# Kernel tuning notes

Hardware: AMD Instinct MI355X
Metric: run time of the kernel (lower is better)

The kernel has to match this reference:

```python
import jax, jax.numpy as jnp
import numpy as np

H = 128          # hidden_dim
L = 4            # num_layers
NUM_RBF = 16
CUTOFF = 10.0
TIME_DIM = 64
B, N = 4, 512


def _lin_init(key, din, dout):
    return jax.random.normal(key, (din, dout), dtype=jnp.float32) * 0.02


def setup_inputs() -> dict:
    key = jax.random.key(0)
    ks = jax.random.split(key, 16)
    x = jax.random.normal(ks[0], (B, N, 3), dtype=jnp.float32) * 3.0  # spread distances over RBF range
    t = jax.random.uniform(ks[1], (B,), dtype=jnp.float32) * 1000.0
    din_msg = 2 * H + NUM_RBF  # 272
    inp = {
        "x": x,
        "t": t,
        "time_w1": _lin_init(ks[2], TIME_DIM, H),
        "time_b1": jnp.zeros((H,), jnp.float32),
        "time_w2": _lin_init(ks[3], H, H),
        "time_b2": jnp.zeros((H,), jnp.float32),
        # stacked per-layer params, leading axis = layer
        "msg_w1": jax.random.normal(ks[4], (L, din_msg, H), jnp.float32) * 0.02,
        "msg_b1": jnp.zeros((L, H), jnp.float32),
        "msg_w2": jax.random.normal(ks[5], (L, H, H), jnp.float32) * 0.02,
        "msg_b2": jnp.zeros((L, H), jnp.float32),
        "cw1": jax.random.normal(ks[6], (L, H, H), jnp.float32) * 0.02,
        "cb1": jnp.zeros((L, H), jnp.float32),
        "cw2": jax.random.normal(ks[7], (L, H, 1), jnp.float32) * 0.02,
        "cb2": jnp.zeros((L, 1), jnp.float32),
    }
    return inp


def _time_embed(t):
    half = TIME_DIM // 2
    freqs = jnp.exp(jnp.arange(half, dtype=jnp.float32) * (-np.log(10000.0) / (half - 1)))
    ang = t[:, None] * freqs[None, :]                    # (B, half)
    return jnp.concatenate([jnp.sin(ang), jnp.cos(ang)], axis=-1)  # (B, TIME_DIM)


def reference(x, t, time_w1, time_b1, time_w2, time_b2,
              msg_w1, msg_b1, msg_w2, msg_b2, cw1, cb1, cw2, cb2):
    silu = jax.nn.silu
    b, n = x.shape[0], x.shape[1]

    te = _time_embed(t)
    t_emb = silu(te @ time_w1 + time_b1) @ time_w2 + time_b2      # (B, H)
    h = jnp.broadcast_to(t_emb[:, None, :], (b, n, H))            # (B, N, H)

    centers = jnp.linspace(0.0, CUTOFF, NUM_RBF)
    width = CUTOFF / NUM_RBF
    coord_updates = jnp.zeros_like(x)

    for l in range(L):
        diff = x[:, None, :, :] - x[:, :, None, :]                # (B,N,N,3), x_j - x_i
        dist = jnp.linalg.norm(diff, axis=-1)                     # (B,N,N)
        edge_mask = (dist < CUTOFF) & (dist > 0)
        rbf = jnp.exp(-((dist[..., None] - centers) ** 2) / (2.0 * width ** 2))  # (B,N,N,R)

        h_i = jnp.broadcast_to(h[:, :, None, :], (b, n, n, H))
        h_j = jnp.broadcast_to(h[:, None, :, :], (b, n, n, H))
        msg_in = jnp.concatenate([h_i, h_j, rbf], axis=-1)        # (B,N,N,2H+R)

        messages = silu(msg_in @ msg_w1[l] + msg_b1[l]) @ msg_w2[l] + msg_b2[l]
        messages = messages * edge_mask[..., None]
        h = h + messages.sum(axis=2)                              # reduce over j

        weights = silu(messages @ cw1[l] + cb1[l]) @ cw2[l] + cb2[l]  # (B,N,N,1)
        weights = weights * edge_mask[..., None]
        directions = diff / (dist[..., None] + 1e-8)
        coord_updates = coord_updates + (weights * directions).sum(axis=2)

    return coord_updates
```

## Files before the change

### kernel.cpp

```cpp
#include <hip/hip_runtime.h>
#include <hip/hip_bf16.h>
#include <math.h>

#define HD 128
#define NN 512
#define BBATCH 4
#define JT 32

typedef __attribute__((ext_vector_type(8))) short bf16x8;
typedef __attribute__((ext_vector_type(4))) float f32x4;
typedef unsigned int uint;
typedef unsigned short ushort;

#define MFMA16 __builtin_amdgcn_mfma_f32_16x16x32_bf16

__device__ __forceinline__ float silu_f(float v) { return v / (1.f + __expf(-v)); }

__device__ __forceinline__ short f2bf(float v) {
    union { __hip_bfloat16 h; short s; } u;
    u.h = __float2bfloat16(v);
    return u.s;
}

__global__ void k_time(const float* __restrict__ t,
                       const float* __restrict__ w1, const float* __restrict__ b1,
                       const float* __restrict__ w2, const float* __restrict__ b2,
                       float* __restrict__ t_emb) {
    int b = blockIdx.x;
    int h = threadIdx.x;
    __shared__ float te[64];
    __shared__ float hid[128];
    float tv = t[b];
    if (h < 32) {
        const float cst = (float)(-2.302585092994046 * 4.0 / 31.0);
        float freq = __expf((float)h * cst);
        float ang = tv * freq;
        te[h]      = sinf(ang);
        te[h + 32] = cosf(ang);
    }
    __syncthreads();
    float acc = b1[h];
    #pragma unroll 8
    for (int k = 0; k < 64; ++k) acc += te[k] * w1[k * HD + h];
    hid[h] = silu_f(acc);
    __syncthreads();
    float acc2 = b2[h];
    #pragma unroll 8
    for (int k = 0; k < HD; ++k) acc2 += hid[k] * w2[k * HD + h];
    t_emb[b * HD + h] = acc2;
}

__global__ void k_bcast(const float* __restrict__ t_emb, float* __restrict__ h,
                        ushort* __restrict__ hb) {
    int idx = blockIdx.x * 256 + threadIdx.x;
    int hch = idx & 127;
    int b = idx >> 16;
    float v = t_emb[b * HD + hch];
    h[idx] = v;
    hb[idx] = (ushort)f2bf(v);
}

__global__ void k_proj(const float* __restrict__ h,
                       const float* __restrict__ w1,
                       const float* __restrict__ b1,
                       float* __restrict__ A) {
    int node = blockIdx.x;
    int hc = threadIdx.x;
    __shared__ float hrow[HD];
    hrow[hc] = h[node * HD + hc];
    __syncthreads();
    float a = b1[hc];
    #pragma unroll 8
    for (int k = 0; k < HD; ++k) a += hrow[k] * w1[k * HD + hc];
    A[node * HD + hc] = a;
}

__global__ __launch_bounds__(256, 2)
void k_edge(const float* __restrict__ x,
            const float* __restrict__ h_in, const ushort* __restrict__ hb_in,
            float* __restrict__ h_out, ushort* __restrict__ hb_out,
            const float* __restrict__ A,
            const float* __restrict__ w1,
            const float* __restrict__ w2,
            const float* __restrict__ b2,
            const float* __restrict__ cw1,
            const float* __restrict__ cb1,
            const float* __restrict__ cw2,
            const float* __restrict__ cb2,
            float* __restrict__ out) {
    __shared__ uint4 sAq[2][JT * 32];
    __shared__ uint4 sMAq[JT * 16];
    __shared__ uint4 sMMq[JT * 16];
    __shared__ __align__(16) float sPart[JT * 68];
    __shared__ float sDir[2][JT][3];
    __shared__ float sMask[2][JT];
    __shared__ float sHS[HD];
    __shared__ float sCA[JT][3];

    const int tid = threadIdx.x;
    const int l  = tid & 63;
    const int w  = tid >> 6;
    const int lg = l >> 4;
    const int ln = l & 15;
    const int nb = w * 32;
    const int n0 = nb + ln;
    const int n1 = n0 + 16;
    const int node = blockIdx.x;
    const int b = node >> 9;
    const float* __restrict__ xb = x + (size_t)b * NN * 3;
    const ushort* __restrict__ hbN = hb_in + (size_t)b * NN * HD;

    const float* w1m = w1 + 128 * HD;
    const float* w1r = w1 + 256 * HD;

    const float bb20 = b2[n0], bb21 = b2[n1];
    const float cb10 = cb1[n0], cb11 = cb1[n1];
    const float cwv0 = cw2[n0], cwv1 = cw2[n1];
    const float cb2v = cb2[0];
    const float xi0 = x[node * 3 + 0], xi1 = x[node * 3 + 1], xi2 = x[node * 3 + 2];
    const float cstep = 10.f / 15.f;
    const float rbfk = 1.28f;

    bf16x8 wM[2][4], w2f[2][4], c1f[2][4], wR[2];
    #pragma unroll
    for (int nt = 0; nt < 2; ++nt) {
        int n = nb + nt * 16 + ln;
        #pragma unroll
        for (int ks = 0; ks < 4; ++ks) {
            #pragma unroll
            for (int i = 0; i < 8; ++i) {
                int k = ks * 32 + lg * 8 + i;
                wM[nt][ks][i]  = f2bf(w1m[k * HD + n]);
                w2f[nt][ks][i] = f2bf(w2[k * HD + n]);
                c1f[nt][ks][i] = f2bf(cw1[k * HD + n]);
            }
        }
        #pragma unroll
        for (int i = 0; i < 8; ++i) {
            int kr = lg * 8 + i;
            float v = (kr < 16) ? w1r[kr * HD + n]
                    : (kr == 16 ? A[node * HD + n] : 0.f);
            wR[nt][i] = f2bf(v);
        }
    }

    if (tid < 64) {
        char* base = (char*)sAq[tid >> 5] + (tid & 31) * 512;
        int sw = ((tid & 7) << 4);
        *(uint*)(base + (288 ^ sw) + 0)  = 0x00003F80u;
        *(uint*)(base + (288 ^ sw) + 4)  = 0u;
        *(uint*)(base + (288 ^ sw) + 8)  = 0u;
        *(uint*)(base + (288 ^ sw) + 12) = 0u;
        uint4 z4 = {0u, 0u, 0u, 0u};
        *(uint4*)(base + (304 ^ sw)) = z4;
    }

    const int hr = tid >> 4, hseg = tid & 15;
    const int jj = tid >> 3, rp = tid & 7;

    {
        char* bufc = (char*)sAq[0];
        const ushort* src = hbN + (size_t)hr * HD + hseg * 8;
        uint4 hv0 = *(const uint4*)src;
        uint4 hv1 = *(const uint4*)(src + 16 * HD);
        const float* xj = xb + jj * 3;
        float d0 = xj[0] - xi0, d1 = xj[1] - xi1, d2 = xj[2] - xi2;
        float d = sqrtf(d0 * d0 + d1 * d1 + d2 * d2);
        float c0 = (float)(rp * 2) * cstep;
        float e0 = __expf(-(d - c0) * (d - c0) * rbfk);
        float e1 = __expf(-(d - c0 - cstep) * (d - c0 - cstep) * rbfk);
        uint pk = (uint)(ushort)f2bf(e0) | ((uint)(ushort)f2bf(e1) << 16);
        *(uint*)(bufc + jj * 512 + ((256 + (rp & 4) * 4) ^ ((jj & 7) << 4)) + (rp & 3) * 4) = pk;
        if (rp == 0) {
            float inv = 1.f / (d + 1e-8f);
            sDir[0][jj][0] = d0 * inv; sDir[0][jj][1] = d1 * inv; sDir[0][jj][2] = d2 * inv;
            sMask[0][jj] = (d < 10.f && d > 0.f) ? 1.f : 0.f;
        }
        int off = (hseg * 16) ^ ((hr & 7) << 4);
        *(uint4*)(bufc + hr * 512 + off) = hv0;
        *(uint4*)(bufc + (hr + 16) * 512 + off) = hv1;
    }
    float hreg0 = 0.f, hreg1 = 0.f;
    float ca0 = 0.f, ca1 = 0.f, ca2 = 0.f;
    __syncthreads();

    const int swA = (ln & 7) << 4;
    const int colb0 = nb * 2 + (ln & 8) * 2 + (ln & 7) * 2;
    const int colb1 = (nb + 16) * 2 + (ln & 8) * 2 + (ln & 7) * 2;

    for (int it = 0; it <= 16; ++it) {
        if (it > 0) {
            const int pm = (it - 1) & 1;
            const char* pp = (const char*)sPart + jj * 272;
            f32x4 pa = *(const f32x4*)(pp + ((jj & 7) << 4 ^ (rp * 32)));
            f32x4 pb = *(const f32x4*)(pp + ((jj & 7) << 4 ^ (rp * 32 + 16)));
            float s = pa[0] + pa[1] + pa[2] + pa[3] + pb[0] + pb[1] + pb[2] + pb[3];
            s += __shfl_xor(s, 1); s += __shfl_xor(s, 2); s += __shfl_xor(s, 4);
            if (rp == 0) {
                float wv = (s + cb2v) * sMask[pm][jj];
                ca0 += wv * sDir[pm][jj][0];
                ca1 += wv * sDir[pm][jj][1];
                ca2 += wv * sDir[pm][jj][2];
            }
        }
        if (it == 16) break;
        const int p = it & 1;

        uint4 hv0, hv1;
        if (it < 15) {
            const ushort* src = hbN + (size_t)((it + 1) * JT + hr) * HD + hseg * 8;
            hv0 = *(const uint4*)src;
            hv1 = *(const uint4*)(src + 16 * HD);
            char* bufn = (char*)sAq[p ^ 1];
            int j = (it + 1) * JT + jj;
            const float* xj = xb + j * 3;
            float d0 = xj[0] - xi0, d1 = xj[1] - xi1, d2 = xj[2] - xi2;
            float d = sqrtf(d0 * d0 + d1 * d1 + d2 * d2);
            float c0 = (float)(rp * 2) * cstep;
            float e0 = __expf(-(d - c0) * (d - c0) * rbfk);
            float e1 = __expf(-(d - c0 - cstep) * (d - c0 - cstep) * rbfk);
            uint pk = (uint)(ushort)f2bf(e0) | ((uint)(ushort)f2bf(e1) << 16);
            *(uint*)(bufn + jj * 512 + ((256 + (rp & 4) * 4) ^ ((jj & 7) << 4)) + (rp & 3) * 4) = pk;
            if (rp == 0) {
                float inv = 1.f / (d + 1e-8f);
                sDir[p ^ 1][jj][0] = d0 * inv; sDir[p ^ 1][jj][1] = d1 * inv; sDir[p ^ 1][jj][2] = d2 * inv;
                sMask[p ^ 1][jj] = (d < 10.f && d > 0.f) ? 1.f : 0.f;
            }
        }

        {
            const char* bufc = (const char*)sAq[p];
            f32x4 zz = {0.f, 0.f, 0.f, 0.f};
            f32x4 pacc[2][2];
            #pragma unroll
            for (int mt = 0; mt < 2; ++mt) {
                pacc[mt][0] = zz; pacc[mt][1] = zz;
                const char* rowp = bufc + (ln + mt * 16) * 512;
                bf16x8 af[5];
                #pragma unroll
                for (int ks = 0; ks < 5; ++ks)
                    af[ks] = *(const bf16x8*)(rowp + ((ks * 64 + lg * 16) ^ swA));
                #pragma unroll
                for (int ks = 0; ks < 4; ++ks) {
                    pacc[mt][0] = MFMA16(af[ks], wM[0][ks], pacc[mt][0], 0, 0, 0);
                    pacc[mt][1] = MFMA16(af[ks], wM[1][ks], pacc[mt][1], 0, 0, 0);
                }
                pacc[mt][0] = MFMA16(af[4], wR[0], pacc[mt][0], 0, 0, 0);
                pacc[mt][1] = MFMA16(af[4], wR[1], pacc[mt][1], 0, 0, 0);
            }
            #pragma unroll
            for (int mt = 0; mt < 2; ++mt)
                #pragma unroll
                for (int reg = 0; reg < 4; ++reg) {
                    int j = mt * 16 + lg * 4 + reg;
                    int sw = (j & 7) << 4;
                    *(short*)((char*)sMAq + j * 256 + (colb0 ^ sw)) = f2bf(silu_f(pacc[mt][0][reg]));
                    *(short*)((char*)sMAq + j * 256 + (colb1 ^ sw)) = f2bf(silu_f(pacc[mt][1][reg]));
                }
        }
        if (it < 15) {
            char* bufn = (char*)sAq[p ^ 1];
            int off = (hseg * 16) ^ ((hr & 7) << 4);
            *(uint4*)(bufn + hr * 512 + off) = hv0;
            *(uint4*)(bufn + (hr + 16) * 512 + off) = hv1;
        }
        __syncthreads();

        {
            f32x4 macc[2][2];
            f32x4 i0 = {bb20, bb20, bb20, bb20};
            f32x4 i1 = {bb21, bb21, bb21, bb21};
            #pragma unroll
            for (int mt = 0; mt < 2; ++mt) {
                macc[mt][0] = i0; macc[mt][1] = i1;
                const char* rowp = (const char*)sMAq + (ln + mt * 16) * 256;
                bf16x8 am[4];
                #pragma unroll
                for (int ks = 0; ks < 4; ++ks)
                    am[ks] = *(const bf16x8*)(rowp + ((ks * 64 + lg * 16) ^ swA));
                #pragma unroll
                for (int ks = 0; ks < 4; ++ks) {
                    macc[mt][0] = MFMA16(am[ks], w2f[0][ks], macc[mt][0], 0, 0, 0);
                    macc[mt][1] = MFMA16(am[ks], w2f[1][ks], macc[mt][1], 0, 0, 0);
                }
            }
            #pragma unroll
            for (int mt = 0; mt < 2; ++mt)
                #pragma unroll
                for (int reg = 0; reg < 4; ++reg) {
                    int j = mt * 16 + lg * 4 + reg;
                    float msk = sMask[p][j];
                    float g0 = macc[mt][0][reg] * msk;
                    float g1 = macc[mt][1][reg] * msk;
                    hreg0 += g0; hreg1 += g1;
                    int sw = (j & 7) << 4;
                    *(short*)((char*)sMMq + j * 256 + (colb0 ^ sw)) = f2bf(g0);
                    *(short*)((char*)sMMq + j * 256 + (colb1 ^ sw)) = f2bf(g1);
                }
        }
        __syncthreads();

        {
            f32x4 cacc[2][2];
            f32x4 i0 = {cb10, cb10, cb10, cb10};
            f32x4 i1 = {cb11, cb11, cb11, cb11};
            #pragma unroll
            for (int mt = 0; mt < 2; ++mt) {
                cacc[mt][0] = i0; cacc[mt][1] = i1;
                const char* rowp = (const char*)sMMq + (ln + mt * 16) * 256;
                bf16x8 am[4];
                #pragma unroll
                for (int ks = 0; ks < 4; ++ks)
                    am[ks] = *(const bf16x8*)(rowp + ((ks * 64 + lg * 16) ^ swA));
                #pragma unroll
                for (int ks = 0; ks < 4; ++ks) {
                    cacc[mt][0] = MFMA16(am[ks], c1f[0][ks], cacc[mt][0], 0, 0, 0);
                    cacc[mt][1] = MFMA16(am[ks], c1f[1][ks], cacc[mt][1], 0, 0, 0);
                }
            }
            #pragma unroll
            for (int mt = 0; mt < 2; ++mt)
                #pragma unroll
                for (int reg = 0; reg < 4; ++reg) {
                    int j = mt * 16 + lg * 4 + reg;
                    float v = silu_f(cacc[mt][0][reg]) * cwv0 + silu_f(cacc[mt][1][reg]) * cwv1;
                    *(float*)((char*)sPart + j * 272 + (((w * 16 + ln) * 4) ^ ((j & 7) << 4))) = v;
                }
        }
        __syncthreads();
    }

    float t0 = hreg0 + __shfl_xor(hreg0, 16); t0 += __shfl_xor(t0, 32);
    float t1 = hreg1 + __shfl_xor(hreg1, 16); t1 += __shfl_xor(t1, 32);
    if (lg == 0) { sHS[n0] = t0; sHS[n1] = t1; }
    if (rp == 0) { sCA[jj][0] = ca0; sCA[jj][1] = ca1; sCA[jj][2] = ca2; }
    __syncthreads();
    if (tid < HD) {
        float hv = h_in[node * HD + tid] + sHS[tid];
        h_out[node * HD + tid] = hv;
        hb_out[node * HD + tid] = (ushort)f2bf(hv);
    }
    if (tid < 3) {
        float s = 0.f;
        #pragma unroll
        for (int q = 0; q < JT; ++q) s += sCA[q][tid];
        out[node * 3 + tid] += s;
    }
}

extern "C" void kernel_launch(void* const* d_in, const int* in_sizes, int n_in,
                              void* d_out, int out_size, void* d_ws, size_t ws_size,
                              hipStream_t stream) {
    const float* x   = (const float*)d_in[0];
    const float* t   = (const float*)d_in[1];
    const float* tw1 = (const float*)d_in[2];
    const float* tb1 = (const float*)d_in[3];
    const float* tw2 = (const float*)d_in[4];
    const float* tb2 = (const float*)d_in[5];
    const float* mw1 = (const float*)d_in[6];
    const float* mb1 = (const float*)d_in[7];
    const float* mw2 = (const float*)d_in[8];
    const float* mb2 = (const float*)d_in[9];
    const float* cw1 = (const float*)d_in[10];
    const float* cb1 = (const float*)d_in[11];
    const float* cw2 = (const float*)d_in[12];
    const float* cb2 = (const float*)d_in[13];
    float* out = (float*)d_out;
    float* ws = (float*)d_ws;

    float* t_emb = ws;
    float* h0 = ws + 512;
    float* h1 = h0 + 262144;
    float* Abuf = h1 + 262144;
    ushort* hb0 = (ushort*)(Abuf + 262144);
    ushort* hb1 = hb0 + 262144;

    hipMemsetAsync(d_out, 0, (size_t)out_size * sizeof(float), stream);
    k_time<<<BBATCH, 128, 0, stream>>>(t, tw1, tb1, tw2, tb2, t_emb);
    k_bcast<<<(BBATCH * NN * HD) / 256, 256, 0, stream>>>(t_emb, h0, hb0);

    float* hc = h0;  ushort* hbc = hb0;
    float* hn = h1;  ushort* hbn = hb1;
    for (int l = 0; l < 4; ++l) {
        k_proj<<<BBATCH * NN, 128, 0, stream>>>(hc, mw1 + (size_t)l * 272 * 128,
                                                mb1 + l * 128, Abuf);
        k_edge<<<BBATCH * NN, 256, 0, stream>>>(
            x, hc, hbc, hn, hbn, Abuf,
            mw1 + (size_t)l * 272 * 128,
            mw2 + (size_t)l * 128 * 128, mb2 + l * 128,
            cw1 + (size_t)l * 128 * 128, cb1 + l * 128,
            cw2 + l * 128, cb2 + l, out);
        float* tf = hc; hc = hn; hn = tf;
        ushort* tb = hbc; hbc = hbn; hbn = tb;
    }
}
```

Baseline: 1.128 ms.

## Precompute per-node h_j projection in k_proj, drop per-edge h_j MFMA

The h_j half of the first message layer is now computed once per node in k_proj, using the same linear split already applied to h_i, and stored as bf16. The edge kernel adds this precomputed term to the small rbf/A MFMA result instead of running four K-steps of MFMA per tile. This removes most of the first-layer edge matmul and the wM weight registers, so shared-memory rows shrink and launch bounds rise to three blocks per CU. It also swaps divisions for hardware reciprocals in silu and the direction normalisation, and introduces extra bf16 rounding of the projected term.

```diff
diff --git a/kernel.cpp b/kernel.cpp
--- a/kernel.cpp
+++ b/kernel.cpp
@@ -6,6 +6,7 @@
 #define NN 512
 #define BBATCH 4
 #define JT 32
+#define APITCH 384
 
 typedef __attribute__((ext_vector_type(8))) short bf16x8;
 typedef __attribute__((ext_vector_type(4))) float f32x4;
@@ -14,7 +15,10 @@
 
 #define MFMA16 __builtin_amdgcn_mfma_f32_16x16x32_bf16
 
-__device__ __forceinline__ float silu_f(float v) { return v / (1.f + __expf(-v)); }
+__device__ __forceinline__ float silu_f(float v) {
+    float e = __expf(-v);
+    return v * __builtin_amdgcn_rcpf(1.f + e);
+}
 
 __device__ __forceinline__ short f2bf(float v) {
     union { __hip_bfloat16 h; short s; } u;
@@ -50,37 +54,38 @@
     t_emb[b * HD + h] = acc2;
 }
 
-__global__ void k_bcast(const float* __restrict__ t_emb, float* __restrict__ h,
-                        ushort* __restrict__ hb) {
+__global__ void k_bcast(const float* __restrict__ t_emb, float* __restrict__ h) {
     int idx = blockIdx.x * 256 + threadIdx.x;
     int hch = idx & 127;
     int b = idx >> 16;
-    float v = t_emb[b * HD + hch];
-    h[idx] = v;
-    hb[idx] = (ushort)f2bf(v);
+    h[idx] = t_emb[b * HD + hch];
 }
 
 __global__ void k_proj(const float* __restrict__ h,
                        const float* __restrict__ w1,
                        const float* __restrict__ b1,
-                       float* __restrict__ A) {
+                       float* __restrict__ A, ushort* __restrict__ Bpb) {
     int node = blockIdx.x;
     int hc = threadIdx.x;
     __shared__ float hrow[HD];
     hrow[hc] = h[node * HD + hc];
     __syncthreads();
     float a = b1[hc];
+    float bb = 0.f;
     #pragma unroll 8
-    for (int k = 0; k < HD; ++k) a += hrow[k] * w1[k * HD + hc];
+    for (int k = 0; k < HD; ++k) {
+        a  += hrow[k] * w1[k * HD + hc];
+        bb += hrow[k] * w1[(HD + k) * HD + hc];
+    }
     A[node * HD + hc] = a;
-}
-
-__global__ __launch_bounds__(256, 2)
+    Bpb[node * HD + hc] = (ushort)f2bf(bb);
+}
+
+__global__ __launch_bounds__(256, 3)
 void k_edge(const float* __restrict__ x,
-            const float* __restrict__ h_in, const ushort* __restrict__ hb_in,
-            float* __restrict__ h_out, ushort* __restrict__ hb_out,
-            const float* __restrict__ A,
-            const float* __restrict__ w1,
+            const float* __restrict__ h_in, float* __restrict__ h_out,
+            const float* __restrict__ A, const ushort* __restrict__ Bpb,
+            const float* __restrict__ w1r,
             const float* __restrict__ w2,
             const float* __restrict__ b2,
             const float* __restrict__ cw1,
@@ -88,7 +93,7 @@
             const float* __restrict__ cw2,
             const float* __restrict__ cb2,
             float* __restrict__ out) {
-    __shared__ uint4 sAq[2][JT * 32];
+    __shared__ uint4 sAq[2][JT * (APITCH / 16)];
     __shared__ uint4 sMAq[JT * 16];
     __shared__ uint4 sMMq[JT * 16];
     __shared__ __align__(16) float sPart[JT * 68];
@@ -108,10 +113,7 @@
     const int node = blockIdx.x;
     const int b = node >> 9;
     const float* __restrict__ xb = x + (size_t)b * NN * 3;
-    const ushort* __restrict__ hbN = hb_in + (size_t)b * NN * HD;
-
-    const float* w1m = w1 + 128 * HD;
-    const float* w1r = w1 + 256 * HD;
+    const ushort* __restrict__ BpbN = Bpb + (size_t)b * NN * HD;
 
     const float bb20 = b2[n0], bb21 = b2[n1];
     const float cb10 = cb1[n0], cb11 = cb1[n1];
@@ -121,7 +123,7 @@
     const float cstep = 10.f / 15.f;
     const float rbfk = 1.28f;
 
-    bf16x8 wM[2][4], w2f[2][4], c1f[2][4], wR[2];
+    bf16x8 wR[2], w2f[2][4], c1f[2][4];
     #pragma unroll
     for (int nt = 0; nt < 2; ++nt) {
         int n = nb + nt * 16 + ln;
@@ -130,7 +132,6 @@
             #pragma unroll
             for (int i = 0; i < 8; ++i) {
                 int k = ks * 32 + lg * 8 + i;
-                wM[nt][ks][i]  = f2bf(w1m[k * HD + n]);
                 w2f[nt][ks][i] = f2bf(w2[k * HD + n]);
                 c1f[nt][ks][i] = f2bf(cw1[k * HD + n]);
             }
@@ -145,7 +146,7 @@
     }
 
     if (tid < 64) {
-        char* base = (char*)sAq[tid >> 5] + (tid & 31) * 512;
+        char* base = (char*)sAq + (tid >> 5) * (JT * APITCH) + (tid & 31) * APITCH;
         int sw = ((tid & 7) << 4);
         *(uint*)(base + (288 ^ sw) + 0)  = 0x00003F80u;
         *(uint*)(base + (288 ^ sw) + 4)  = 0u;
@@ -159,10 +160,10 @@
     const int jj = tid >> 3, rp = tid & 7;
 
     {
-        char* bufc = (char*)sAq[0];
-        const ushort* src = hbN + (size_t)hr * HD + hseg * 8;
-        uint4 hv0 = *(const uint4*)src;
-        uint4 hv1 = *(const uint4*)(src + 16 * HD);
+        char* bufc = (char*)sAq;
+        const ushort* src = BpbN + (size_t)hr * HD + hseg * 8;
+        uint4 bv0 = *(const uint4*)src;
+        uint4 bv1 = *(const uint4*)(src + 16 * HD);
         const float* xj = xb + jj * 3;
         float d0 = xj[0] - xi0, d1 = xj[1] - xi1, d2 = xj[2] - xi2;
         float d = sqrtf(d0 * d0 + d1 * d1 + d2 * d2);
@@ -170,15 +171,15 @@
         float e0 = __expf(-(d - c0) * (d - c0) * rbfk);
         float e1 = __expf(-(d - c0 - cstep) * (d - c0 - cstep) * rbfk);
         uint pk = (uint)(ushort)f2bf(e0) | ((uint)(ushort)f2bf(e1) << 16);
-        *(uint*)(bufc + jj * 512 + ((256 + (rp & 4) * 4) ^ ((jj & 7) << 4)) + (rp & 3) * 4) = pk;
+        *(uint*)(bufc + jj * APITCH + ((256 + (rp & 4) * 4) ^ ((jj & 7) << 4)) + (rp & 3) * 4) = pk;
         if (rp == 0) {
-            float inv = 1.f / (d + 1e-8f);
+            float inv = __builtin_amdgcn_rcpf(d + 1e-8f);
             sDir[0][jj][0] = d0 * inv; sDir[0][jj][1] = d1 * inv; sDir[0][jj][2] = d2 * inv;
             sMask[0][jj] = (d < 10.f && d > 0.f) ? 1.f : 0.f;
         }
         int off = (hseg * 16) ^ ((hr & 7) << 4);
-        *(uint4*)(bufc + hr * 512 + off) = hv0;
-        *(uint4*)(bufc + (hr + 16) * 512 + off) = hv1;
+        *(uint4*)(bufc + hr * APITCH + off) = bv0;
+        *(uint4*)(bufc + (hr + 16) * APITCH + off) = bv1;
     }
     float hreg0 = 0.f, hreg1 = 0.f;
     float ca0 = 0.f, ca1 = 0.f, ca2 = 0.f;
@@ -206,12 +207,12 @@
         if (it == 16) break;
         const int p = it & 1;
 
-        uint4 hv0, hv1;
+        uint4 bv0, bv1;
         if (it < 15) {
-            const ushort* src = hbN + (size_t)((it + 1) * JT + hr) * HD + hseg * 8;
-            hv0 = *(const uint4*)src;
-            hv1 = *(const uint4*)(src + 16 * HD);
-            char* bufn = (char*)sAq[p ^ 1];
+            const ushort* src = BpbN + (size_t)((it + 1) * JT + hr) * HD + hseg * 8;
+            bv0 = *(const uint4*)src;
+            bv1 = *(const uint4*)(src + 16 * HD);
+            char* bufn = (char*)sAq + (p ^ 1) * (JT * APITCH);
             int j = (it + 1) * JT + jj;
             const float* xj = xb + j * 3;
             float d0 = xj[0] - xi0, d1 = xj[1] - xi1, d2 = xj[2] - xi2;
@@ -220,49 +221,42 @@
             float e0 = __expf(-(d - c0) * (d - c0) * rbfk);
             float e1 = __expf(-(d - c0 - cstep) * (d - c0 - cstep) * rbfk);
             uint pk = (uint)(ushort)f2bf(e0) | ((uint)(ushort)f2bf(e1) << 16);
-            *(uint*)(bufn + jj * 512 + ((256 + (rp & 4) * 4) ^ ((jj & 7) << 4)) + (rp & 3) * 4) = pk;
+            *(uint*)(bufn + jj * APITCH + ((256 + (rp & 4) * 4) ^ ((jj & 7) << 4)) + (rp & 3) * 4) = pk;
             if (rp == 0) {
-                float inv = 1.f / (d + 1e-8f);
+                float inv = __builtin_amdgcn_rcpf(d + 1e-8f);
                 sDir[p ^ 1][jj][0] = d0 * inv; sDir[p ^ 1][jj][1] = d1 * inv; sDir[p ^ 1][jj][2] = d2 * inv;
                 sMask[p ^ 1][jj] = (d < 10.f && d > 0.f) ? 1.f : 0.f;
             }
         }
 
         {
-            const char* bufc = (const char*)sAq[p];
+            const char* bufc = (const char*)sAq + p * (JT * APITCH);
             f32x4 zz = {0.f, 0.f, 0.f, 0.f};
-            f32x4 pacc[2][2];
             #pragma unroll
             for (int mt = 0; mt < 2; ++mt) {
-                pacc[mt][0] = zz; pacc[mt][1] = zz;
-                const char* rowp = bufc + (ln + mt * 16) * 512;
-                bf16x8 af[5];
-                #pragma unroll
-                for (int ks = 0; ks < 5; ++ks)
-                    af[ks] = *(const bf16x8*)(rowp + ((ks * 64 + lg * 16) ^ swA));
-                #pragma unroll
-                for (int ks = 0; ks < 4; ++ks) {
-                    pacc[mt][0] = MFMA16(af[ks], wM[0][ks], pacc[mt][0], 0, 0, 0);
-                    pacc[mt][1] = MFMA16(af[ks], wM[1][ks], pacc[mt][1], 0, 0, 0);
-                }
-                pacc[mt][0] = MFMA16(af[4], wR[0], pacc[mt][0], 0, 0, 0);
-                pacc[mt][1] = MFMA16(af[4], wR[1], pacc[mt][1], 0, 0, 0);
-            }
-            #pragma unroll
-            for (int mt = 0; mt < 2; ++mt)
+                const char* rowp = bufc + (ln + mt * 16) * APITCH;
+                bf16x8 af4 = *(const bf16x8*)(rowp + ((256 + lg * 16) ^ swA));
+                f32x4 p0 = MFMA16(af4, wR[0], zz, 0, 0, 0);
+                f32x4 p1 = MFMA16(af4, wR[1], zz, 0, 0, 0);
                 #pragma unroll
                 for (int reg = 0; reg < 4; ++reg) {
                     int j = mt * 16 + lg * 4 + reg;
                     int sw = (j & 7) << 4;
-                    *(short*)((char*)sMAq + j * 256 + (colb0 ^ sw)) = f2bf(silu_f(pacc[mt][0][reg]));
-                    *(short*)((char*)sMAq + j * 256 + (colb1 ^ sw)) = f2bf(silu_f(pacc[mt][1][reg]));
-                }
+                    const char* brow = bufc + j * APITCH;
+                    uint u0 = *(const ushort*)(brow + (colb0 ^ sw));
+                    uint u1 = *(const ushort*)(brow + (colb1 ^ sw));
+                    float v0 = silu_f(p0[reg] + __uint_as_float(u0 << 16));
+                    float v1 = silu_f(p1[reg] + __uint_as_float(u1 << 16));
+                    *(short*)((char*)sMAq + j * 256 + (colb0 ^ sw)) = f2bf(v0);
+                    *(short*)((char*)sMAq + j * 256 + (colb1 ^ sw)) = f2bf(v1);
+                }
+            }
         }
         if (it < 15) {
-            char* bufn = (char*)sAq[p ^ 1];
+            char* bufn = (char*)sAq + (p ^ 1) * (JT * APITCH);
             int off = (hseg * 16) ^ ((hr & 7) << 4);
-            *(uint4*)(bufn + hr * 512 + off) = hv0;
-            *(uint4*)(bufn + (hr + 16) * 512 + off) = hv1;
+            *(uint4*)(bufn + hr * APITCH + off) = bv0;
+            *(uint4*)(bufn + (hr + 16) * APITCH + off) = bv1;
         }
         __syncthreads();
 
@@ -330,16 +324,12 @@
         __syncthreads();
     }
 
-    float t0 = hreg0 + __shfl_xor(hreg0, 16); t0 += __shfl_xor(t0, 32);
-    float t1 = hreg1 + __shfl_xor(hreg1, 16); t1 += __shfl_xor(t1, 32);
-    if (lg == 0) { sHS[n0] = t0; sHS[n1] = t1; }
+    float t0 = hreg0; t0 += __shfl_xor(t0, 16); t0 += __shfl_xor(t0, 32);
+    float t1 = hreg1; t1 += __shfl_xor(t1, 16); t1 += __shfl_xor(t1, 32);
+    if (l < 16) { sHS[n0] = t0; sHS[n1] = t1; }
     if (rp == 0) { sCA[jj][0] = ca0; sCA[jj][1] = ca1; sCA[jj][2] = ca2; }
     __syncthreads();
-    if (tid < HD) {
-        float hv = h_in[node * HD + tid] + sHS[tid];
-        h_out[node * HD + tid] = hv;
-        hb_out[node * HD + tid] = (ushort)f2bf(hv);
-    }
+    if (tid < HD) h_out[node * HD + tid] = h_in[node * HD + tid] + sHS[tid];
     if (tid < 3) {
         float s = 0.f;
         #pragma unroll
@@ -372,25 +362,23 @@
     float* h0 = ws + 512;
     float* h1 = h0 + 262144;
     float* Abuf = h1 + 262144;
-    ushort* hb0 = (ushort*)(Abuf + 262144);
-    ushort* hb1 = hb0 + 262144;
+    ushort* Bpb = (ushort*)(Abuf + 262144);
 
     hipMemsetAsync(d_out, 0, (size_t)out_size * sizeof(float), stream);
     k_time<<<BBATCH, 128, 0, stream>>>(t, tw1, tb1, tw2, tb2, t_emb);
-    k_bcast<<<(BBATCH * NN * HD) / 256, 256, 0, stream>>>(t_emb, h0, hb0);
-
-    float* hc = h0;  ushort* hbc = hb0;
-    float* hn = h1;  ushort* hbn = hb1;
+    k_bcast<<<(BBATCH * NN * HD) / 256, 256, 0, stream>>>(t_emb, h0);
+
+    float* hc = h0;
+    float* hn = h1;
     for (int l = 0; l < 4; ++l) {
         k_proj<<<BBATCH * NN, 128, 0, stream>>>(hc, mw1 + (size_t)l * 272 * 128,
-                                                mb1 + l * 128, Abuf);
+                                                mb1 + l * 128, Abuf, Bpb);
         k_edge<<<BBATCH * NN, 256, 0, stream>>>(
-            x, hc, hbc, hn, hbn, Abuf,
-            mw1 + (size_t)l * 272 * 128,
+            x, hc, hn, Abuf, Bpb,
+            mw1 + (size_t)l * 272 * 128 + 256 * 128,
             mw2 + (size_t)l * 128 * 128, mb2 + l * 128,
             cw1 + (size_t)l * 128 * 128, cb1 + l * 128,
             cw2 + l * 128, cb2 + l, out);
         float* tf = hc; hc = hn; hn = tf;
-        ushort* tb = hbc; hbc = hbn; hbn = tb;
-    }
-}
+    }
+}
```

After: 2.475 ms. 2.19x slower.
